# Optimization experiments

Hardware: AMD Instinct MI355X
Metric: run time of the kernel (lower is better)

The kernel has to match this reference:

```python
import jax, jax.numpy as jnp
import numpy as np

C = 256
EPS = 1e-5


def setup_inputs() -> dict:
    key = jax.random.key(0)
    ks = jax.random.split(key, 10)
    B, H, W = 4, 64, 64
    x1 = jax.random.normal(ks[0], (B, C, H, W), dtype=jnp.float32)
    x2 = jax.random.normal(ks[1], (B, C, H, W), dtype=jnp.float32)
    s = 1.0 / np.sqrt(C)
    qw = jax.random.normal(ks[2], (C, C), dtype=jnp.float32) * s
    qb = jax.random.normal(ks[3], (C,), dtype=jnp.float32) * 0.01
    kw = jax.random.normal(ks[4], (C, C), dtype=jnp.float32) * s
    kb = jax.random.normal(ks[5], (C,), dtype=jnp.float32) * 0.01
    vw = jax.random.normal(ks[6], (C, C), dtype=jnp.float32) * s
    vb = jax.random.normal(ks[7], (C,), dtype=jnp.float32) * 0.01
    ln_w = jnp.ones((C,), dtype=jnp.float32)
    ln_b = jnp.zeros((C,), dtype=jnp.float32)
    return {"x1": x1, "x2": x2, "qw": qw, "qb": qb, "kw": kw, "kb": kb,
            "vw": vw, "vb": vb, "ln_w": ln_w, "ln_b": ln_b}


def _conv1x1(x, w, b):
    # 1x1 conv == per-pixel matmul over channels. x: [B,C,H,W], w: [O,C]
    return jnp.einsum('oc,bchw->bohw', w, x) + b[None, :, None, None]


def reference(x1, x2, qw, qb, kw, kb, vw, vb, ln_w, ln_b):
    q = _conv1x1(x1, qw, qb)   # [B,C,H,W]
    k = _conv1x1(x2, kw, kb)   # [B,C,H,W]
    v = _conv1x1(x2, vw, vb)   # [B,C,H,W]
    # scores: [B,H,W,I,J]; softmax over LAST axis (j) only, as in the torch code
    scores = jnp.einsum('bchw,bcij->bhwij', q, k)
    attn = jax.nn.softmax(scores, axis=-1)
    fusion = jnp.einsum('bhwij,bcij->bchw', attn, v)  # [B,C,H,W]
    # LayerNorm2d: normalize over channel dim per spatial location
    mean = jnp.mean(fusion, axis=1, keepdims=True)
    var = jnp.var(fusion, axis=1, keepdims=True)
    normed = (fusion - mean) * jax.lax.rsqrt(var + EPS)
    return normed * ln_w[None, :, None, None] + ln_b[None, :, None, None]
```

## Files before the change

### kernel.cpp

```cpp
#include <hip/hip_runtime.h>


#define CDIM 256
#define NPOS 4096
#define BATCH 4
#define EPSV 1e-5f

typedef _Float16 f16;
typedef __attribute__((ext_vector_type(8))) _Float16 f16x8;
typedef __attribute__((ext_vector_type(4))) float f32x4;
typedef __attribute__((ext_vector_type(16))) float f32x16;

#define QK_STRIDE 264
#define V_STRIDE  72
#define S_STRIDE  68
#define P_STRIDE  72
#define DS_V_STRIDE 72


static __device__ __forceinline__ f16x8 cvt8(const float* __restrict__ p) {
    float4 w0 = *(const float4*)p;
    float4 w1 = *(const float4*)(p + 4);
    f16x8 r;
    r[0] = (f16)w0.x; r[1] = (f16)w0.y; r[2] = (f16)w0.z; r[3] = (f16)w0.w;
    r[4] = (f16)w1.x; r[5] = (f16)w1.y; r[6] = (f16)w1.z; r[7] = (f16)w1.w;
    return r;
}

__global__ __launch_bounds__(256, 4) void prep_kernel(
    const float* __restrict__ x1, const float* __restrict__ x2,
    const float* __restrict__ qw, const float* __restrict__ kw,
    const float* __restrict__ vw,
    f16* __restrict__ X1T, f16* __restrict__ X2T, f16* __restrict__ W16)
{
    const int id = blockIdx.x;
    const int t  = threadIdx.x;
    if (id < 2048) {
        __shared__ f16 T[64 * 72];
        const float* xs = (id & 1) ? x2 : x1;
        f16* dst        = (id & 1) ? X2T : X1T;
        const int t2 = id >> 1;
        const int b  = t2 >> 8;
        const int rm = t2 & 255;
        const int c0 = (rm >> 6) * 64;
        const int n0 = (rm & 63) * 64;
        const float* src = xs + ((size_t)b * CDIM + c0) * NPOS + n0;
        const int rr = t >> 6, col = t & 63;
        #pragma unroll
        for (int j = 0; j < 16; ++j) {
            int row = rr + j * 4;
            T[col * 72 + row] = (f16)src[(size_t)row * NPOS + col];
        }
        __syncthreads();
        const int n = t >> 3, lc = (t & 7) * 8;
        f16* d0 = dst + ((size_t)b * NPOS + n0) * CDIM + c0;
        #pragma unroll
        for (int j = 0; j < 2; ++j) {
            int nn = n + j * 32;
            *(f16x8*)(d0 + (size_t)nn * CDIM + lc) = *(const f16x8*)&T[nn * 72 + lc];
        }
    } else {
        const int wblk = id - 2048;
        const int pr = wblk >> 2, h = wblk & 3;
        const float* W = (pr == 0 ? qw : pr == 1 ? kw : vw) + (size_t)h * 64 * CDIM;
        f16* D = W16 + (size_t)pr * CDIM * CDIM + (size_t)h * 64 * CDIM;
        #pragma unroll
        for (int i = 0; i < 8; ++i) {
            int g = t + i * 256;
            int row = g >> 5, col = (g & 31) * 8;
            *(f16x8*)(D + (size_t)row * CDIM + col) = cvt8(W + (size_t)row * CDIM + col);
        }
    }
}

__global__ __launch_bounds__(256, 2) void gemm_kernel(
    const f16* __restrict__ X1T, const f16* __restrict__ X2T,
    const f16* __restrict__ W16,
    const float* __restrict__ qb, const float* __restrict__ kb,
    const float* __restrict__ vb,
    f16* __restrict__ Qg, f16* __restrict__ Kg, f16* __restrict__ Vg)
{
    __shared__ f16 Xs[64 * QK_STRIDE];
    __shared__ f16 Ds[256 * 72];
    __shared__ float biasS[256];

    const int id = blockIdx.x;
    const int pr  = id >> 8;
    const int rem = id & 255;
    const int b   = rem >> 6;
    const int p0  = (rem & 63) << 6;
    const f16* XT = (pr == 0) ? X1T : X2T;
    const f16* Wp = W16 + (size_t)pr * CDIM * CDIM;
    const float* bias = pr == 0 ? qb : pr == 1 ? kb : vb;

    const int t = threadIdx.x, w = t >> 6, l = t & 63, lm = l & 31, lh = l >> 5;

    biasS[t] = bias[t];
    #pragma unroll
    for (int it = 0; it < 8; ++it) {
        int p = w * 16 + it * 2 + lh;
        *(f16x8*)&Xs[p * QK_STRIDE + lm * 8] =
            *(const f16x8*)(XT + ((size_t)(b * NPOS + p0 + p)) * CDIM + lm * 8);
    }
    __syncthreads();

    f32x16 acc[2][2] = {};
    for (int ks = 0; ks < 16; ++ks) {
        f16x8 x0 = *(const f16x8*)&Xs[lm * QK_STRIDE + ks * 16 + lh * 8];
        f16x8 x1v = *(const f16x8*)&Xs[(32 + lm) * QK_STRIDE + ks * 16 + lh * 8];
        f16x8 w0 = *(const f16x8*)(Wp + (size_t)(w * 64 + lm) * CDIM + ks * 16 + lh * 8);
        f16x8 w1 = *(const f16x8*)(Wp + (size_t)(w * 64 + 32 + lm) * CDIM + ks * 16 + lh * 8);
        if (pr < 2) {
            acc[0][0] = __builtin_amdgcn_mfma_f32_32x32x16_f16(x0, w0, acc[0][0], 0, 0, 0);
            acc[0][1] = __builtin_amdgcn_mfma_f32_32x32x16_f16(x0, w1, acc[0][1], 0, 0, 0);
            acc[1][0] = __builtin_amdgcn_mfma_f32_32x32x16_f16(x1v, w0, acc[1][0], 0, 0, 0);
            acc[1][1] = __builtin_amdgcn_mfma_f32_32x32x16_f16(x1v, w1, acc[1][1], 0, 0, 0);
        } else {
            acc[0][0] = __builtin_amdgcn_mfma_f32_32x32x16_f16(w0, x0, acc[0][0], 0, 0, 0);
            acc[0][1] = __builtin_amdgcn_mfma_f32_32x32x16_f16(w0, x1v, acc[0][1], 0, 0, 0);
            acc[1][0] = __builtin_amdgcn_mfma_f32_32x32x16_f16(w1, x0, acc[1][0], 0, 0, 0);
            acc[1][1] = __builtin_amdgcn_mfma_f32_32x32x16_f16(w1, x1v, acc[1][1], 0, 0, 0);
        }
    }

    if (pr < 2) {
        #pragma unroll
        for (int pt = 0; pt < 2; ++pt)
            #pragma unroll
            for (int oi = 0; oi < 2; ++oi) {
                int oc = w * 64 + oi * 32 + lm;
                float bv = biasS[oc];
                #pragma unroll
                for (int r = 0; r < 16; ++r) {
                    int p = pt * 32 + (r & 3) + 8 * (r >> 2) + 4 * lh;
                    Ds[p * QK_STRIDE + oc] = (f16)(acc[pt][oi][r] + bv);
                }
            }
        __syncthreads();
        f16* Out = (pr == 0) ? Qg : Kg;
        #pragma unroll
        for (int it = 0; it < 8; ++it) {
            int p = w * 16 + it * 2 + lh;
            *(f16x8*)(Out + ((size_t)(b * NPOS + p0 + p)) * CDIM + lm * 8) =
                *(const f16x8*)&Ds[p * QK_STRIDE + lm * 8];
        }
    } else {
        #pragma unroll
        for (int oi = 0; oi < 2; ++oi)
            #pragma unroll
            for (int pt = 0; pt < 2; ++pt) {
                #pragma unroll
                for (int r = 0; r < 16; ++r) {
                    int ol = oi * 32 + (r & 3) + 8 * (r >> 2) + 4 * lh;
                    Ds[(w * 64 + ol) * DS_V_STRIDE + pt * 32 + lm] =
                        (f16)(acc[oi][pt][r] + biasS[w * 64 + ol]);
                }
            }
        __syncthreads();
        #pragma unroll
        for (int it = 0; it < 8; ++it) {
            int ol = it * 8 + (l >> 3);
            int cl = (l & 7) * 8;
            *(f16x8*)(Vg + ((size_t)(b * CDIM + w * 64 + ol)) * NPOS + p0 + cl) =
                *(const f16x8*)&Ds[(w * 64 + ol) * DS_V_STRIDE + cl];
        }
    }
}

__global__ __launch_bounds__(256, 1) void attn_kernel(
    const f16* __restrict__ Qg, const f16* __restrict__ Kg, const f16* __restrict__ Vg,
    const float* __restrict__ ln_w, const float* __restrict__ ln_b,
    float* __restrict__ out)
{
    __shared__ f16   Ks[64 * QK_STRIDE];
    __shared__ f16   Vs[256 * V_STRIDE];
    __shared__ float Ss[64 * S_STRIDE];
    __shared__ f16   Ps[64 * P_STRIDE];
    __shared__ float lnw_s[256], lnb_s[256];
    __shared__ float redS[4 * 64], redQ[4 * 64], mu_s[64], rs_s[64];

    const int t  = threadIdx.x;
    const int b  = blockIdx.x >> 6;
    const int p0 = (blockIdx.x & 63) << 6;
    const int w  = t >> 6;
    const int l  = t & 63;
    const int lm = l & 31;
    const int lh = l >> 5;

    lnw_s[t] = ln_w[t];
    lnb_s[t] = ln_b[t];

    const int spt = w & 1;
    const int skt = w >> 1;

    f16x8 qf[16];
    {
        const f16* qptr = Qg + (size_t)(b * NPOS + p0 + spt * 32 + lm) * CDIM + lh * 8;
        #pragma unroll
        for (int ks = 0; ks < 16; ++ks) qf[ks] = *(const f16x8*)(qptr + ks * 16);
    }

    const int kr = t >> 5, koff = (t & 31) * 8;
    const int vr = t >> 3, voff = (t & 7) * 8;
    f16x8 kreg[8], vreg[8];
    auto issue_loads = [&](int ch) {
        const int i0 = ch * 64;
        #pragma unroll
        for (int r = 0; r < 8; ++r)
            kreg[r] = *(const f16x8*)(Kg + (size_t)(b * NPOS + i0 + r * 8 + kr) * CDIM + koff);
        #pragma unroll
        for (int r = 0; r < 8; ++r)
            vreg[r] = *(const f16x8*)(Vg + (size_t)(b * CDIM + r * 32 + vr) * NPOS + i0 + voff);
    };
    issue_loads(0);

    f32x16 facc[4] = {};

    for (int ch = 0; ch < 64; ++ch) {
        #pragma unroll
        for (int r = 0; r < 8; ++r)
            *(f16x8*)&Ks[(r * 8 + kr) * QK_STRIDE + koff] = kreg[r];
        __syncthreads();

        #pragma unroll
        for (int r = 0; r < 8; ++r)
            *(f16x8*)&Vs[(r * 32 + vr) * V_STRIDE + voff] = vreg[r];

        f32x16 sacc = {};
        for (int ks = 0; ks < 16; ++ks) {
            f16x8 bb = *(const f16x8*)&Ks[(skt * 32 + lm) * QK_STRIDE + ks * 16 + lh * 8];
            sacc = __builtin_amdgcn_mfma_f32_32x32x16_f16(qf[ks], bb, sacc, 0, 0, 0);
        }
        #pragma unroll
        for (int r = 0; r < 16; ++r) {
            int row = (r & 3) + 8 * (r >> 2) + 4 * lh;
            Ss[(spt * 32 + row) * S_STRIDE + skt * 32 + lm] = sacc[r];
        }
        __syncthreads();

        {
            const int r  = t >> 2;
            const int sg = (t & 3) * 16;
            const float* srow = &Ss[r * S_STRIDE + sg];
            float v[16];
            f32x4 a0 = *(const f32x4*)(srow);
            f32x4 a1 = *(const f32x4*)(srow + 4);
            f32x4 a2 = *(const f32x4*)(srow + 8);
            f32x4 a3 = *(const f32x4*)(srow + 12);
            v[0]=a0[0]; v[1]=a0[1]; v[2]=a0[2]; v[3]=a0[3];
            v[4]=a1[0]; v[5]=a1[1]; v[6]=a1[2]; v[7]=a1[3];
            v[8]=a2[0]; v[9]=a2[1]; v[10]=a2[2]; v[11]=a2[3];
            v[12]=a3[0]; v[13]=a3[1]; v[14]=a3[2]; v[15]=a3[3];
            float m = v[0];
            #pragma unroll
            for (int i = 1; i < 16; ++i) m = fmaxf(m, v[i]);
            m = fmaxf(m, __shfl_xor(m, 1));
            m = fmaxf(m, __shfl_xor(m, 2));
            float s = 0.f;
            #pragma unroll
            for (int i = 0; i < 16; ++i) { float e = __expf(v[i] - m); v[i] = e; s += e; }
            s += __shfl_xor(s, 1);
            s += __shfl_xor(s, 2);
            float inv = __builtin_amdgcn_rcpf(s);
            f16x8 h0, h1;
            #pragma unroll
            for (int i = 0; i < 8; ++i) { h0[i] = (f16)(v[i] * inv); h1[i] = (f16)(v[i + 8] * inv); }
            *(f16x8*)&Ps[r * P_STRIDE + sg]     = h0;
            *(f16x8*)&Ps[r * P_STRIDE + sg + 8] = h1;
        }
        __syncthreads();

        if (ch < 63) issue_loads(ch + 1);

        #pragma unroll
        for (int ks = 0; ks < 4; ++ks) {
            f16x8 bp0 = *(const f16x8*)&Ps[lm * P_STRIDE + ks * 16 + lh * 8];
            f16x8 bp1 = *(const f16x8*)&Ps[(32 + lm) * P_STRIDE + ks * 16 + lh * 8];
            f16x8 av0 = *(const f16x8*)&Vs[(w * 64 + lm) * V_STRIDE + ks * 16 + lh * 8];
            f16x8 av1 = *(const f16x8*)&Vs[(w * 64 + 32 + lm) * V_STRIDE + ks * 16 + lh * 8];
            facc[0] = __builtin_amdgcn_mfma_f32_32x32x16_f16(av0, bp0, facc[0], 0, 0, 0);
            facc[1] = __builtin_amdgcn_mfma_f32_32x32x16_f16(av0, bp1, facc[1], 0, 0, 0);
            facc[2] = __builtin_amdgcn_mfma_f32_32x32x16_f16(av1, bp0, facc[2], 0, 0, 0);
            facc[3] = __builtin_amdgcn_mfma_f32_32x32x16_f16(av1, bp1, facc[3], 0, 0, 0);
        }
    }

    float ps0 = 0.f, ps1 = 0.f, pq0 = 0.f, pq1 = 0.f;
    #pragma unroll
    for (int ii = 0; ii < 2; ++ii) {
        #pragma unroll
        for (int r = 0; r < 16; ++r) {
            float a = facc[ii * 2 + 0][r];
            float c = facc[ii * 2 + 1][r];
            ps0 += a; pq0 += a * a;
            ps1 += c; pq1 += c * c;
        }
    }
    ps0 += __shfl_xor(ps0, 32); pq0 += __shfl_xor(pq0, 32);
    ps1 += __shfl_xor(ps1, 32); pq1 += __shfl_xor(pq1, 32);
    if (lh == 0) {
        redS[w * 64 + lm] = ps0;        redQ[w * 64 + lm] = pq0;
        redS[w * 64 + 32 + lm] = ps1;   redQ[w * 64 + 32 + lm] = pq1;
    }
    __syncthreads();
    if (t < 64) {
        float s = redS[t] + redS[64 + t] + redS[128 + t] + redS[192 + t];
        float q = redQ[t] + redQ[64 + t] + redQ[128 + t] + redQ[192 + t];
        float mean = s * (1.0f / 256.0f);
        float var  = q * (1.0f / 256.0f) - mean * mean;
        mu_s[t] = mean;
        rs_s[t] = rsqrtf(var + EPSV);
    }
    __syncthreads();
    #pragma unroll
    for (int ii = 0; ii < 2; ++ii) {
        #pragma unroll
        for (int jj = 0; jj < 2; ++jj) {
            int p = jj * 32 + lm;
            float mu = mu_s[p], rs = rs_s[p];
            float* dst = out + (size_t)b * CDIM * NPOS + p0 + p;
            #pragma unroll
            for (int r = 0; r < 16; ++r) {
                int c = w * 64 + ii * 32 + (r & 3) + 8 * (r >> 2) + 4 * lh;
                float vL = facc[ii * 2 + jj][r];
                dst[(size_t)c * NPOS] = (vL - mu) * rs * lnw_s[c] + lnb_s[c];
            }
        }
    }
}

extern "C" void kernel_launch(void* const* d_in, const int* in_sizes, int n_in,
                              void* d_out, int out_size, void* d_ws, size_t ws_size,
                              hipStream_t stream)
{
    const float* x1  = (const float*)d_in[0];
    const float* x2  = (const float*)d_in[1];
    const float* qw  = (const float*)d_in[2];
    const float* qb  = (const float*)d_in[3];
    const float* kw  = (const float*)d_in[4];
    const float* kb  = (const float*)d_in[5];
    const float* vw  = (const float*)d_in[6];
    const float* vb  = (const float*)d_in[7];
    const float* lnw = (const float*)d_in[8];
    const float* lnb = (const float*)d_in[9];

    const size_t tsz = (size_t)BATCH * NPOS * CDIM;
    f16* Qg  = (f16*)d_ws;
    f16* Kg  = Qg + tsz;
    f16* Vg  = Kg + tsz;
    f16* X1T = Vg + tsz;
    f16* X2T = X1T + tsz;
    f16* W16 = X2T + tsz;

    prep_kernel<<<2060, 256, 0, stream>>>(x1, x2, qw, kw, vw, X1T, X2T, W16);
    gemm_kernel<<<768, 256, 0, stream>>>(X1T, X2T, W16, qb, kb, vb, Qg, Kg, Vg);
    attn_kernel<<<256, 256, 0, stream>>>(Qg, Kg, Vg, lnw, lnb, (float*)d_out);
}
```

Baseline: 242.9 us.

## Stage weights in LDS for projection GEMM and load V fragments directly in attention

The projection GEMM now stages each 64-row weight slice in shared memory and loops over four output slices, each wave computing one 32x32 tile with two split-K accumulators. This replaces per-wave global weight reads and shrinks the output staging buffer. The attention kernel drops the shared-memory V tile and has each wave load its V MFMA fragments straight from global memory, which frees LDS so it can launch with two blocks per CU. The cost is more syncs in the GEMM and uncoalesced 16-byte V loads issued inside the loop, whose latency may be exposed.

```diff
diff --git a/kernel.cpp b/kernel.cpp
--- a/kernel.cpp
+++ b/kernel.cpp
@@ -11,11 +11,11 @@
 typedef __attribute__((ext_vector_type(4))) float f32x4;
 typedef __attribute__((ext_vector_type(16))) float f32x16;
 
+#define WST       264
 #define QK_STRIDE 264
-#define V_STRIDE  72
 #define S_STRIDE  68
 #define P_STRIDE  72
-#define DS_V_STRIDE 72
+#define DQ_STRIDE 72
 
 
 static __device__ __forceinline__ f16x8 cvt8(const float* __restrict__ p) {
@@ -80,8 +80,9 @@
     const float* __restrict__ vb,
     f16* __restrict__ Qg, f16* __restrict__ Kg, f16* __restrict__ Vg)
 {
-    __shared__ f16 Xs[64 * QK_STRIDE];
-    __shared__ f16 Ds[256 * 72];
+    __shared__ f16 Xs[64 * WST];
+    __shared__ f16 Wh[64 * WST];
+    __shared__ f16 Ds[64 * DQ_STRIDE];
     __shared__ float biasS[256];
 
     const int id = blockIdx.x;
@@ -94,86 +95,81 @@
     const float* bias = pr == 0 ? qb : pr == 1 ? kb : vb;
 
     const int t = threadIdx.x, w = t >> 6, l = t & 63, lm = l & 31, lh = l >> 5;
+    const int pt = w & 1, ot = w >> 1;
 
     biasS[t] = bias[t];
     #pragma unroll
     for (int it = 0; it < 8; ++it) {
         int p = w * 16 + it * 2 + lh;
-        *(f16x8*)&Xs[p * QK_STRIDE + lm * 8] =
+        *(f16x8*)&Xs[p * WST + lm * 8] =
             *(const f16x8*)(XT + ((size_t)(b * NPOS + p0 + p)) * CDIM + lm * 8);
     }
-    __syncthreads();
-
-    f32x16 acc[2][2] = {};
-    for (int ks = 0; ks < 16; ++ks) {
-        f16x8 x0 = *(const f16x8*)&Xs[lm * QK_STRIDE + ks * 16 + lh * 8];
-        f16x8 x1v = *(const f16x8*)&Xs[(32 + lm) * QK_STRIDE + ks * 16 + lh * 8];
-        f16x8 w0 = *(const f16x8*)(Wp + (size_t)(w * 64 + lm) * CDIM + ks * 16 + lh * 8);
-        f16x8 w1 = *(const f16x8*)(Wp + (size_t)(w * 64 + 32 + lm) * CDIM + ks * 16 + lh * 8);
+
+    for (int q = 0; q < 4; ++q) {
+        #pragma unroll
+        for (int i = 0; i < 8; ++i) {
+            int g = t + i * 256;
+            int row = g >> 5, col = (g & 31) * 8;
+            *(f16x8*)&Wh[row * WST + col] =
+                *(const f16x8*)(Wp + (size_t)(q * 64 + row) * CDIM + col);
+        }
+        __syncthreads();
+
+        f32x16 accA = {}, accB = {};
+        #pragma unroll
+        for (int ks = 0; ks < 16; ks += 2) {
+            f16x8 x0 = *(const f16x8*)&Xs[(pt * 32 + lm) * WST + ks * 16 + lh * 8];
+            f16x8 w0 = *(const f16x8*)&Wh[(ot * 32 + lm) * WST + ks * 16 + lh * 8];
+            f16x8 x1v = *(const f16x8*)&Xs[(pt * 32 + lm) * WST + (ks + 1) * 16 + lh * 8];
+            f16x8 w1 = *(const f16x8*)&Wh[(ot * 32 + lm) * WST + (ks + 1) * 16 + lh * 8];
+            if (pr < 2) {
+                accA = __builtin_amdgcn_mfma_f32_32x32x16_f16(x0, w0, accA, 0, 0, 0);
+                accB = __builtin_amdgcn_mfma_f32_32x32x16_f16(x1v, w1, accB, 0, 0, 0);
+            } else {
+                accA = __builtin_amdgcn_mfma_f32_32x32x16_f16(w0, x0, accA, 0, 0, 0);
+                accB = __builtin_amdgcn_mfma_f32_32x32x16_f16(w1, x1v, accB, 0, 0, 0);
+            }
+        }
+
         if (pr < 2) {
-            acc[0][0] = __builtin_amdgcn_mfma_f32_32x32x16_f16(x0, w0, acc[0][0], 0, 0, 0);
-            acc[0][1] = __builtin_amdgcn_mfma_f32_32x32x16_f16(x0, w1, acc[0][1], 0, 0, 0);
-            acc[1][0] = __builtin_amdgcn_mfma_f32_32x32x16_f16(x1v, w0, acc[1][0], 0, 0, 0);
-            acc[1][1] = __builtin_amdgcn_mfma_f32_32x32x16_f16(x1v, w1, acc[1][1], 0, 0, 0);
+            int o_l = ot * 32 + lm;
+            float bv = biasS[q * 64 + o_l];
+            #pragma unroll
+            for (int r = 0; r < 16; ++r) {
+                int p_l = pt * 32 + (r & 3) + 8 * (r >> 2) + 4 * lh;
+                Ds[p_l * DQ_STRIDE + o_l] = (f16)(accA[r] + accB[r] + bv);
+            }
         } else {
-            acc[0][0] = __builtin_amdgcn_mfma_f32_32x32x16_f16(w0, x0, acc[0][0], 0, 0, 0);
-            acc[0][1] = __builtin_amdgcn_mfma_f32_32x32x16_f16(w0, x1v, acc[0][1], 0, 0, 0);
-            acc[1][0] = __builtin_amdgcn_mfma_f32_32x32x16_f16(w1, x0, acc[1][0], 0, 0, 0);
-            acc[1][1] = __builtin_amdgcn_mfma_f32_32x32x16_f16(w1, x1v, acc[1][1], 0, 0, 0);
-        }
-    }
-
-    if (pr < 2) {
-        #pragma unroll
-        for (int pt = 0; pt < 2; ++pt)
-            #pragma unroll
-            for (int oi = 0; oi < 2; ++oi) {
-                int oc = w * 64 + oi * 32 + lm;
-                float bv = biasS[oc];
-                #pragma unroll
-                for (int r = 0; r < 16; ++r) {
-                    int p = pt * 32 + (r & 3) + 8 * (r >> 2) + 4 * lh;
-                    Ds[p * QK_STRIDE + oc] = (f16)(acc[pt][oi][r] + bv);
-                }
-            }
-        __syncthreads();
-        f16* Out = (pr == 0) ? Qg : Kg;
-        #pragma unroll
-        for (int it = 0; it < 8; ++it) {
-            int p = w * 16 + it * 2 + lh;
-            *(f16x8*)(Out + ((size_t)(b * NPOS + p0 + p)) * CDIM + lm * 8) =
-                *(const f16x8*)&Ds[p * QK_STRIDE + lm * 8];
-        }
-    } else {
-        #pragma unroll
-        for (int oi = 0; oi < 2; ++oi)
-            #pragma unroll
-            for (int pt = 0; pt < 2; ++pt) {
-                #pragma unroll
-                for (int r = 0; r < 16; ++r) {
-                    int ol = oi * 32 + (r & 3) + 8 * (r >> 2) + 4 * lh;
-                    Ds[(w * 64 + ol) * DS_V_STRIDE + pt * 32 + lm] =
-                        (f16)(acc[oi][pt][r] + biasS[w * 64 + ol]);
-                }
-            }
-        __syncthreads();
-        #pragma unroll
-        for (int it = 0; it < 8; ++it) {
-            int ol = it * 8 + (l >> 3);
-            int cl = (l & 7) * 8;
-            *(f16x8*)(Vg + ((size_t)(b * CDIM + w * 64 + ol)) * NPOS + p0 + cl) =
-                *(const f16x8*)&Ds[(w * 64 + ol) * DS_V_STRIDE + cl];
-        }
-    }
-}
-
-__global__ __launch_bounds__(256, 1) void attn_kernel(
+            #pragma unroll
+            for (int r = 0; r < 16; ++r) {
+                int o_l = ot * 32 + (r & 3) + 8 * (r >> 2) + 4 * lh;
+                Ds[o_l * DQ_STRIDE + pt * 32 + lm] =
+                    (f16)(accA[r] + accB[r] + biasS[q * 64 + o_l]);
+            }
+        }
+        __syncthreads();
+
+        #pragma unroll
+        for (int j = 0; j < 2; ++j) {
+            int row = (t >> 3) + j * 32;
+            int cc  = (t & 7) * 8;
+            f16x8 vdat = *(const f16x8*)&Ds[row * DQ_STRIDE + cc];
+            if (pr < 2) {
+                f16* Out = (pr == 0) ? Qg : Kg;
+                *(f16x8*)(Out + ((size_t)(b * NPOS + p0 + row)) * CDIM + q * 64 + cc) = vdat;
+            } else {
+                *(f16x8*)(Vg + ((size_t)(b * CDIM + q * 64 + row)) * NPOS + p0 + cc) = vdat;
+            }
+        }
+    }
+}
+
+__global__ __launch_bounds__(256, 2) void attn_kernel(
     const f16* __restrict__ Qg, const f16* __restrict__ Kg, const f16* __restrict__ Vg,
     const float* __restrict__ ln_w, const float* __restrict__ ln_b,
     float* __restrict__ out)
 {
     __shared__ f16   Ks[64 * QK_STRIDE];
-    __shared__ f16   Vs[256 * V_STRIDE];
     __shared__ float Ss[64 * S_STRIDE];
     __shared__ f16   Ps[64 * P_STRIDE];
     __shared__ float lnw_s[256], lnb_s[256];
@@ -201,32 +197,36 @@
     }
 
     const int kr = t >> 5, koff = (t & 31) * 8;
-    const int vr = t >> 3, voff = (t & 7) * 8;
-    f16x8 kreg[8], vreg[8];
-    auto issue_loads = [&](int ch) {
+    f16x8 kreg[8];
+    auto issue_k = [&](int ch) {
         const int i0 = ch * 64;
         #pragma unroll
         for (int r = 0; r < 8; ++r)
             kreg[r] = *(const f16x8*)(Kg + (size_t)(b * NPOS + i0 + r * 8 + kr) * CDIM + koff);
-        #pragma unroll
-        for (int r = 0; r < 8; ++r)
-            vreg[r] = *(const f16x8*)(Vg + (size_t)(b * CDIM + r * 32 + vr) * NPOS + i0 + voff);
     };
-    issue_loads(0);
+    issue_k(0);
+
+    const f16* vbase0 = Vg + (size_t)(b * CDIM + w * 64 + lm) * NPOS;
+    const f16* vbase1 = Vg + (size_t)(b * CDIM + w * 64 + 32 + lm) * NPOS;
 
     f32x16 facc[4] = {};
 
     for (int ch = 0; ch < 64; ++ch) {
+        const int i0 = ch * 64;
         #pragma unroll
         for (int r = 0; r < 8; ++r)
             *(f16x8*)&Ks[(r * 8 + kr) * QK_STRIDE + koff] = kreg[r];
         __syncthreads();
 
-        #pragma unroll
-        for (int r = 0; r < 8; ++r)
-            *(f16x8*)&Vs[(r * 32 + vr) * V_STRIDE + voff] = vreg[r];
+        f16x8 vf0[4], vf1[4];
+        #pragma unroll
+        for (int ks = 0; ks < 4; ++ks) {
+            vf0[ks] = *(const f16x8*)(vbase0 + i0 + ks * 16 + lh * 8);
+            vf1[ks] = *(const f16x8*)(vbase1 + i0 + ks * 16 + lh * 8);
+        }
 
         f32x16 sacc = {};
+        #pragma unroll
         for (int ks = 0; ks < 16; ++ks) {
             f16x8 bb = *(const f16x8*)&Ks[(skt * 32 + lm) * QK_STRIDE + ks * 16 + lh * 8];
             sacc = __builtin_amdgcn_mfma_f32_32x32x16_f16(qf[ks], bb, sacc, 0, 0, 0);
@@ -270,18 +270,16 @@
         }
         __syncthreads();
 
-        if (ch < 63) issue_loads(ch + 1);
+        if (ch < 63) issue_k(ch + 1);
 
         #pragma unroll
         for (int ks = 0; ks < 4; ++ks) {
             f16x8 bp0 = *(const f16x8*)&Ps[lm * P_STRIDE + ks * 16 + lh * 8];
             f16x8 bp1 = *(const f16x8*)&Ps[(32 + lm) * P_STRIDE + ks * 16 + lh * 8];
-            f16x8 av0 = *(const f16x8*)&Vs[(w * 64 + lm) * V_STRIDE + ks * 16 + lh * 8];
-            f16x8 av1 = *(const f16x8*)&Vs[(w * 64 + 32 + lm) * V_STRIDE + ks * 16 + lh * 8];
-            facc[0] = __builtin_amdgcn_mfma_f32_32x32x16_f16(av0, bp0, facc[0], 0, 0, 0);
-            facc[1] = __builtin_amdgcn_mfma_f32_32x32x16_f16(av0, bp1, facc[1], 0, 0, 0);
-            facc[2] = __builtin_amdgcn_mfma_f32_32x32x16_f16(av1, bp0, facc[2], 0, 0, 0);
-            facc[3] = __builtin_amdgcn_mfma_f32_32x32x16_f16(av1, bp1, facc[3], 0, 0, 0);
+            facc[0] = __builtin_amdgcn_mfma_f32_32x32x16_f16(vf0[ks], bp0, facc[0], 0, 0, 0);
+            facc[1] = __builtin_amdgcn_mfma_f32_32x32x16_f16(vf0[ks], bp1, facc[1], 0, 0, 0);
+            facc[2] = __builtin_amdgcn_mfma_f32_32x32x16_f16(vf1[ks], bp0, facc[2], 0, 0, 0);
+            facc[3] = __builtin_amdgcn_mfma_f32_32x32x16_f16(vf1[ks], bp1, facc[3], 0, 0, 0);
         }
     }
 
```

After: 248.2 us. 2.2% more time.
